# Optimization experiments

Measured on AMD Instinct MI355X. Metric: run time of the kernel, lower is better.

The kernel has to match this reference:

```python
import math
import jax, jax.numpy as jnp
import numpy as np

B, N, D, H, PQ, PV = 2, 2048, 256, 8, 4, 8
HD = D // H
OUT_IN = D + H * PV * 3 + H  # 256 + 192 + 8 = 456


def setup_inputs() -> dict:
    key = jax.random.key(0)
    ks = jax.random.split(key, 12)
    w = lambda k, shape: (jax.random.normal(k, shape, jnp.float32) * 0.02)
    return {
        "x": jax.random.normal(ks[0], (B, N, D), jnp.float32),
        "rotations": jax.random.normal(ks[1], (B, N, 3, 3), jnp.float32),
        "translations": jax.random.normal(ks[2], (B, N, 3), jnp.float32),
        "mask": jnp.ones((B, N), dtype=bool),
        "Wq": w(ks[3], (D, D)), "bq": jnp.zeros((D,), jnp.float32),
        "Wk": w(ks[4], (D, D)), "bk": jnp.zeros((D,), jnp.float32),
        "Wv": w(ks[5], (D, D)), "bv": jnp.zeros((D,), jnp.float32),
        "Wo": w(ks[6], (OUT_IN, D)), "bo": jnp.zeros((D,), jnp.float32),
        "head_weights": jnp.ones((H,), jnp.float32),
    }


def reference(x, rotations, translations, mask, Wq, bq, Wk, bk, Wv, bv, Wo, bo, head_weights):
    b, n, d = x.shape
    h = head_weights.shape[0]
    hd = d // h
    pv3 = Wo.shape[0] - d - h  # num_heads * num_value_points * 3

    q = (x @ Wq + bq).reshape(b, n, h, hd)
    k = (x @ Wk + bk).reshape(b, n, h, hd)
    v = (x @ Wv + bv).reshape(b, n, h, hd)

    # scalar attention logits [b,h,i,j]
    attn_scores = jnp.einsum("bihd,bjhd->bhij", q, k) / math.sqrt(hd)

    # point-distance bias from frame translations (rotated q/k/v points are
    # dead code in the original module and are omitted)
    diff = translations[:, :, None, :] - translations[:, None, :, :]  # [b,i,j,3]
    dist_sq = jnp.sum(diff * diff, axis=-1)                            # [b,i,j]
    point_attn = -0.5 * dist_sq[:, None, :, :]                         # [b,1,i,j]

    weights = jax.nn.softmax(head_weights)                             # [h]
    combined = attn_scores + point_attn * weights[None, :, None, None]
    combined = jnp.where(mask[:, None, None, :], combined, -1e9)
    attn_probs = jax.nn.softmax(combined, axis=-1)                     # [b,h,i,j]

    attn_output = jnp.einsum("bhij,bjhd->bihd", attn_probs, v).reshape(b, n, d)

    # translation-weighted points, brought back to local frame
    trans_weighted = jnp.einsum("bhij,bjc->bihc", attn_probs, translations)  # [b,i,h,3]
    trans_local = trans_weighted - translations[:, :, None, :]
    point_out = trans_local.reshape(b, n, h * 3)
    point_out = jnp.pad(point_out, ((0, 0), (0, 0), (0, pv3 - h * 3)))

    mean_dist = jnp.sqrt(jnp.mean(dist_sq, axis=-1, keepdims=True) + 1e-8)  # [b,n,1]
    pair_features = jnp.broadcast_to(mean_dist, (b, n, h))

    output = jnp.concatenate([attn_output, point_out, pair_features], axis=-1)
    return output @ Wo + bo
```

## Files before the change

### kernel.cpp

```cpp
#include <hip/hip_runtime.h>

typedef unsigned short u16;
typedef __attribute__((ext_vector_type(8))) short bf16x8;
typedef __attribute__((ext_vector_type(4))) float f32x4;
typedef __attribute__((ext_vector_type(16))) float f32x16;
typedef __attribute__((ext_vector_type(4))) unsigned u32x4;

#define NB 2
#define NSEQ 2048
#define DD 256
#define NH 8
#define NTOK 4096
#define KF 288
#define KFP 296
#define NSPLIT 4
#define PS 36
#define TSTR 2048

#define L_V 1024
#define L_A 2048
#define L_U 3072
#define L_ZP 3328
#define L_STR 3344

#define SCL2E 0.25506973f
#define L2E 1.4426950408889634f

__device__ __forceinline__ u16 f2b(float f) {
  unsigned u = __builtin_bit_cast(unsigned, f);
  return (u16)((u + 0x7fffu + ((u >> 16) & 1u)) >> 16);
}

__device__ __forceinline__ unsigned cvt_pk_bf16(float lo, float hi) {
  unsigned r;
  asm("v_cvt_pk_bf16_f32 %0, %1, %2" : "=v"(r) : "v"(lo), "v"(hi));
  return r;
}

__device__ __forceinline__ void permlane32_swap(unsigned& a, unsigned& b) {
  asm volatile("v_permlane32_swap_b32 %0, %1" : "+v"(a), "+v"(b));
}

__device__ __forceinline__ f32x4 mfma16(bf16x8 a, bf16x8 b, f32x4 c) {
  return __builtin_amdgcn_mfma_f32_16x16x32_bf16(a, b, c, 0, 0, 0);
}
__device__ __forceinline__ f32x16 mfma32(bf16x8 a, bf16x8 b, f32x16 c) {
  return __builtin_amdgcn_mfma_f32_32x32x16_bf16(a, b, c, 0, 0, 0);
}

#define PB_XB 1024
#define PB_WT (PB_XB + 264)
#define PB_BS (PB_WT + 2)
#define PB_T4 (PB_BS + 16)
#define PB_UC (PB_T4 + 128)
#define PB_AC (PB_UC + 64)
#define PB_N  (PB_AC + 1)
__global__ __launch_bounds__(256) void prep(
    const float* __restrict__ x, const float* __restrict__ tr,
    const float* __restrict__ hw, const float* __restrict__ bq,
    const float* __restrict__ bk, const float* __restrict__ bv,
    const float* __restrict__ Wq, const float* __restrict__ Wk,
    const float* __restrict__ Wv, const float* __restrict__ Wo,
    u16* __restrict__ xb, u16* __restrict__ WqkvT, u16* __restrict__ WoPT,
    float4* __restrict__ t4, float4* __restrict__ bstat,
    u16* __restrict__ UC, u16* __restrict__ AC,
    float* __restrict__ b_all, float* __restrict__ wsoft) {
  __shared__ float lt[32][33];
  __shared__ float4 red[4];
  const int bid = blockIdx.x, t = threadIdx.x;
  if (bid < PB_XB) {
    const int i4 = bid * 256 + t;
    float4 v = *(const float4*)(x + (size_t)i4 * 4);
    ushort4 o;
    o.x = f2b(v.x); o.y = f2b(v.y); o.z = f2b(v.z); o.w = f2b(v.w);
    *(ushort4*)(xb + (size_t)i4 * 4) = o;
  } else if (bid < PB_WT) {
    const int bw = bid - PB_XB;
    const int r = t >> 3, c4 = (t & 7) * 4;
    if (bw < 192) {
      int mt = bw >> 3, kt = bw & 7;
      int m0 = mt * 32, k0 = kt * 32;
      const float* W = m0 < 256 ? Wq : (m0 < 512 ? Wk : Wv);
      const int mm = m0 & 255;
      float4 v = *(const float4*)(W + (size_t)(k0 + r) * 256 + mm + c4);
      lt[r][c4] = v.x; lt[r][c4 + 1] = v.y; lt[r][c4 + 2] = v.z; lt[r][c4 + 3] = v.w;
      __syncthreads();
      const float s = m0 < 256 ? SCL2E : 1.f;
      ushort4 o;
      o.x = f2b(lt[c4][r] * s); o.y = f2b(lt[c4 + 1][r] * s);
      o.z = f2b(lt[c4 + 2][r] * s); o.w = f2b(lt[c4 + 3][r] * s);
      *(ushort4*)(WqkvT + (size_t)(m0 + r) * 256 + k0 + c4) = o;
    } else {
      int q = bw - 192;
      int nt2 = q / 9, kt = q - nt2 * 9;
      int n0 = nt2 * 32, kk0 = kt * 32;
      int row = (kk0 + r) < 280 ? (kk0 + r) : (kk0 + r + 168);
      float4 v = *(const float4*)(Wo + (size_t)row * 256 + n0 + c4);
      lt[r][c4] = v.x; lt[r][c4 + 1] = v.y; lt[r][c4 + 2] = v.z; lt[r][c4 + 3] = v.w;
      __syncthreads();
      ushort4 o;
      o.x = f2b(lt[c4][r]); o.y = f2b(lt[c4 + 1][r]);
      o.z = f2b(lt[c4 + 2][r]); o.w = f2b(lt[c4 + 3][r]);
      *(ushort4*)(WoPT + (size_t)(n0 + r) * KF + kk0 + c4) = o;
    }
  } else if (bid < PB_BS) {
    const int b = bid - PB_WT;
    float sx = 0.f, sy = 0.f, sz = 0.f, s2 = 0.f;
    for (int j = t; j < NSEQ; j += 256) {
      float a = tr[(size_t)(b * NSEQ + j) * 3];
      float b2 = tr[(size_t)(b * NSEQ + j) * 3 + 1];
      float c = tr[(size_t)(b * NSEQ + j) * 3 + 2];
      sx += a; sy += b2; sz += c; s2 += a * a + b2 * b2 + c * c;
    }
#pragma unroll
    for (int off = 1; off < 64; off <<= 1) {
      sx += __shfl_xor(sx, off); sy += __shfl_xor(sy, off);
      sz += __shfl_xor(sz, off); s2 += __shfl_xor(s2, off);
    }
    if ((t & 63) == 0) red[t >> 6] = make_float4(sx, sy, sz, s2);
    __syncthreads();
    if (t == 0) {
      float4 a = red[0], b1 = red[1], c = red[2], d = red[3];
      bstat[b] = make_float4(a.x + b1.x + c.x + d.x, a.y + b1.y + c.y + d.y,
                             a.z + b1.z + c.z + d.z, a.w + b1.w + c.w + d.w);
    }
  } else if (bid < PB_T4) {
    const int j = (bid - PB_BS) * 256 + t;
    float a = tr[j * 3], b2 = tr[j * 3 + 1], c = tr[j * 3 + 2];
    t4[j] = make_float4(a, b2, c, a * a + b2 * b2 + c * c);
  } else if (bid < PB_UC) {
    const int id = (bid - PB_T4) * 256 + t;
    const int b = id >> 14, jt = (id >> 8) & 63, c = (id >> 3) & 31, e = id & 7;
    const int tok = b * NSEQ + jt * 32 + c;
    float v = 0.f;
    if (e < 3) v = tr[(size_t)tok * 3 + e];
    else if (e == 3) {
      float a = tr[(size_t)tok * 3], b2 = tr[(size_t)tok * 3 + 1],
            cz = tr[(size_t)tok * 3 + 2];
      v = a * a + b2 * b2 + cz * cz;
    } else if (e == 4) v = 1.f;
    UC[id] = f2b(v);
  } else if (bid < PB_AC) {
    const int id = (bid - PB_UC) * 256 + t;
    const int b = id >> 13, jt = (id >> 7) & 63, sub = (id >> 5) & 3,
              cch = (id >> 3) & 3, e = id & 7;
    const int j = jt * 32 + (sub >> 1) * 16 + (sub & 1) * 8 + e;
    float v = cch == 0 ? 1.f : tr[(size_t)(b * NSEQ + j) * 3 + cch - 1];
    AC[id] = f2b(v);
  } else {
    for (int i = t; i < 768; i += 256)
      b_all[i] = i < 256 ? bq[i] * SCL2E : i < 512 ? bk[i - 256] : bv[i - 512];
    if (t == 0) {
      float mx = hw[0];
      for (int i = 1; i < NH; i++) mx = fmaxf(mx, hw[i]);
      float e[NH], sum = 0.f;
      for (int i = 0; i < NH; i++) { e[i] = __expf(hw[i] - mx); sum += e[i]; }
      for (int i = 0; i < NH; i++) wsoft[i] = e[i] / sum;
    }
  }
}

__global__ __launch_bounds__(256) void gemm_qkv(
    const u16* __restrict__ AT, const u16* __restrict__ BT,
    const float* __restrict__ bias, u16* __restrict__ Qb,
    u16* __restrict__ TLB) {
  __shared__ u16 vt[128][65];
  const int lane = threadIdx.x & 63, wv = threadIdx.x >> 6;
  const int il = lane & 15, g = lane >> 4;
  const int wm = wv >> 1, wn = wv & 1;
  const int yb = blockIdx.y;
  const int mblk = yb * 64 + wm * 32;
  const int nblk = blockIdx.x * 128 + wn * 64;
  f32x4 acc[2][4];
#pragma unroll
  for (int a = 0; a < 2; a++)
#pragma unroll
    for (int b = 0; b < 4; b++) acc[a][b] = (f32x4)(0.f);
  const u16* Abase = AT + (size_t)(mblk + il) * DD + 8 * g;
  const u16* Bbase = BT + (size_t)(nblk + il) * DD + 8 * g;
#pragma unroll
  for (int kk = 0; kk < DD; kk += 32) {
    bf16x8 aF[2], bF[4];
#pragma unroll
    for (int mt = 0; mt < 2; mt++)
      aF[mt] = *(const bf16x8*)(Abase + (size_t)mt * 16 * DD + kk);
#pragma unroll
    for (int nt = 0; nt < 4; nt++)
      bF[nt] = *(const bf16x8*)(Bbase + (size_t)nt * 16 * DD + kk);
#pragma unroll
    for (int mt = 0; mt < 2; mt++)
#pragma unroll
      for (int nt = 0; nt < 4; nt++)
        acc[mt][nt] = mfma16(aF[mt], bF[nt], acc[mt][nt]);
  }
#pragma unroll
  for (int nt = 0; nt < 4; nt++) {
    const int n_g = nblk + nt * 16 + il;
#pragma unroll
    for (int mt = 0; mt < 2; mt++) {
      const int m0 = mblk + mt * 16 + 4 * g;
      f32x4 v = acc[mt][nt];
      const float4 bb = *(const float4*)(bias + m0);
      v[0] += bb.x; v[1] += bb.y; v[2] += bb.z; v[3] += bb.w;
      ushort4 u;
      u.x = f2b(v[0]); u.y = f2b(v[1]); u.z = f2b(v[2]); u.w = f2b(v[3]);
      if (yb < 4) {
        *(ushort4*)(Qb + (size_t)n_g * 256 + m0) = u;
      } else if (yb < 8) {
        const int f = m0 - 256;
        const int h = f >> 5, dd = (f & 31) >> 3, e0 = f & 7;
        const int b = n_g >> 11, jj = n_g & 2047;
        const int jt = jj >> 5, c = jj & 31;
        u16* tile = TLB + ((size_t)((b * NH + h) * 64 + jt)) * TSTR;
        *(ushort4*)(tile + (size_t)(dd * 32 + c) * 8 + e0) = u;
      } else {
        const int ml = m0 - yb * 64;
        const int nl = wn * 64 + nt * 16 + il;
        vt[nl][ml] = u.x; vt[nl][ml + 1] = u.y;
        vt[nl][ml + 2] = u.z; vt[nl][ml + 3] = u.w;
      }
    }
  }
  if (yb >= 8) {
    __syncthreads();
#pragma unroll
    for (int ii = 0; ii < 4; ++ii) {
      const int q = threadIdx.x + 256 * ii;
      const int jt_loc = q >> 8, qq = q & 255;
      const int sub = qq >> 6, h_loc = (qq >> 5) & 1, c = qq & 31;
      const int jjb = (sub >> 1) * 16 + (sub & 1) * 8;
      const int row0 = jt_loc * 32 + jjb;
      u16 ov[8];
#pragma unroll
      for (int e = 0; e < 8; e++) ov[e] = vt[row0 + e][h_loc * 32 + c];
      const int tok = blockIdx.x * 128 + row0;
      const int b = tok >> 11, jj = tok & 2047, jt = jj >> 5;
      const int h = (yb - 8) * 2 + h_loc;
      u16* tile = TLB + ((size_t)((b * NH + h) * 64 + jt)) * TSTR + L_V;
      *(bf16x8*)(tile + sub * 256 + c * 8) = *(bf16x8*)ov;
    }
  }
}

__global__ __launch_bounds__(256, 4) void attn_kernel(
    const u16* __restrict__ Qb, const u16* __restrict__ TLB,
    const u16* __restrict__ UC, const u16* __restrict__ AC,
    const float4* __restrict__ t4, const float* __restrict__ wsoft,
    float* __restrict__ part) {
  __shared__ __align__(16) u16 lds[2 * L_STR];
  const int tid = threadIdx.x;
  const int lane = tid & 63, wv = tid >> 6;
  const int c = lane & 31, hi = lane >> 5;
  const int bid = blockIdx.x;
  const int idx = bid >> 3;
  const int c2 = (bid & 7) * 8 + (idx >> 4);
  const int bh = c2 >> 2, s = c2 & 3;
  const int b = bh >> 3, h = bh & 7;
  const int qb = (idx & 15) * 128 + wv * 32;
  const int iglob = b * NSEQ + qb + c;

  const u16* qptr = Qb + (size_t)iglob * 256 + h * 32 + 8 * hi;
  const bf16x8 qf0 = *(const bf16x8*)qptr;
  const bf16x8 qf1 = *(const bf16x8*)(qptr + 16);
  const float4 ti = t4[iglob];
  const float w = wsoft[h];
  const float WD = w * L2E, NH2 = -0.5f * WD;
  u32x4 vw = (u32x4)(0u);
  if (hi == 0) {
    vw[0] = cvt_pk_bf16(WD * ti.x, WD * ti.y);
    vw[1] = cvt_pk_bf16(WD * ti.z, NH2);
    vw[2] = cvt_pk_bf16(NH2 * ti.w, 0.f);
  }
  const bf16x8 vf = __builtin_bit_cast(bf16x8, vw);

  f32x16 o = (f32x16)(0.f), aacc = (f32x16)(0.f);
  const int jt0 = s * 16;
  const u16* tK = TLB + ((size_t)bh * 64 + jt0) * TSTR;
  const u16* tA = AC + ((size_t)b * 64 + jt0) * 128;
  const u16* tU = UC + ((size_t)b * 64 + jt0) * 256;
  const int fo = hi * 256 + c * 8;

  {
    unsigned* zz = (unsigned*)lds;
    for (int i = tid; i < 1296; i += 256) {
      int k = (i < 648) ? (L_A / 2 + i) : (L_STR / 2 + L_A / 2 + i - 648);
      zz[k] = 0;
    }
  }
  __syncthreads();
  bf16x8 gkv = *(const bf16x8*)(tK + (size_t)tid * 8);
  bf16x8 ga, gu;
  if (tid < 16) ga = *(const bf16x8*)(tA + tid * 8);
  else if (tid < 48) gu = *(const bf16x8*)(tU + (tid - 16) * 8);
  *(bf16x8*)(lds + tid * 8) = gkv;
  if (tid < 16) *(bf16x8*)(lds + L_A + (tid >> 2) * 256 + (tid & 3) * 8) = ga;
  else if (tid < 48) *(bf16x8*)(lds + L_U + (tid - 16) * 8) = gu;
  __syncthreads();

#pragma unroll 1
  for (int t = 0; t < 16; ++t) {
    if (t < 15) {
      gkv = *(const bf16x8*)(tK + (size_t)(t + 1) * TSTR + tid * 8);
      if (tid < 16) ga = *(const bf16x8*)(tA + (size_t)(t + 1) * 128 + tid * 8);
      else if (tid < 48)
        gu = *(const bf16x8*)(tU + (size_t)(t + 1) * 256 + (tid - 16) * 8);
    }
    const u16* L = lds + (t & 1) * L_STR;
    bf16x8 k0 = *(const bf16x8*)(L + fo);
    bf16x8 k1 = *(const bf16x8*)(L + 512 + fo);
    bf16x8 v0 = *(const bf16x8*)(L + L_V + fo);
    bf16x8 v1 = *(const bf16x8*)(L + L_V + 512 + fo);
    bf16x8 a0 = *(const bf16x8*)(L + L_A + fo);
    bf16x8 a1 = *(const bf16x8*)(L + L_A + 512 + fo);
    bf16x8 uf = *(const bf16x8*)(hi ? (L + L_ZP) : (L + L_U + c * 8));
    __builtin_amdgcn_s_setprio(1);
    f32x16 sa = mfma32(uf, vf, (f32x16)(0.f));
    sa = mfma32(k0, qf0, sa);
    sa = mfma32(k1, qf1, sa);
    float p[16];
#pragma unroll
    for (int r = 0; r < 16; r++) p[r] = exp2f(sa[r]);
    unsigned x0 = cvt_pk_bf16(p[0], p[1]), y0 = cvt_pk_bf16(p[4], p[5]);
    unsigned z0 = cvt_pk_bf16(p[2], p[3]), w0 = cvt_pk_bf16(p[6], p[7]);
    permlane32_swap(x0, y0);
    permlane32_swap(z0, w0);
    unsigned x1 = cvt_pk_bf16(p[8], p[9]), y1 = cvt_pk_bf16(p[12], p[13]);
    unsigned z1 = cvt_pk_bf16(p[10], p[11]), w1 = cvt_pk_bf16(p[14], p[15]);
    permlane32_swap(x1, y1);
    permlane32_swap(z1, w1);
    bf16x8 pa0 = __builtin_bit_cast(bf16x8, (u32x4){x0, z0, y0, w0});
    bf16x8 pa1 = __builtin_bit_cast(bf16x8, (u32x4){x1, z1, y1, w1});
    o = mfma32(pa0, v0, o);
    o = mfma32(pa1, v1, o);
    aacc = mfma32(pa0, a0, aacc);
    aacc = mfma32(pa1, a1, aacc);
    __builtin_amdgcn_s_setprio(0);
    if (t < 15) {
      u16* D = lds + ((t + 1) & 1) * L_STR;
      *(bf16x8*)(D + tid * 8) = gkv;
      if (tid < 16) *(bf16x8*)(D + L_A + (tid >> 2) * 256 + (tid & 3) * 8) = ga;
      else if (tid < 48) *(bf16x8*)(D + L_U + (tid - 16) * 8) = gu;
    }
    __syncthreads();
  }

  float* pbase = part + ((size_t)(s * 16 + bh) * NSEQ + qb) * PS;
#pragma unroll
  for (int r = 0; r < 16; r++) {
    const int irow = (r & 3) + 8 * (r >> 2) + 4 * hi;
    float* pr = pbase + (size_t)irow * PS;
    pr[c] = o[r];
    if (c < 4) pr[32 + c] = aacc[r];
  }
}

__global__ __launch_bounds__(256) void outk(
    const float* __restrict__ part, const u16* __restrict__ WoPT,
    const float* __restrict__ bo, const float4* __restrict__ t4,
    const float4* __restrict__ bstat, const float* __restrict__ tr,
    float* __restrict__ out) {
  __shared__ __align__(16) u16 feats[16][KFP];
  __shared__ float invl[16][8];
  const int t = threadIdx.x;
  const int tok0 = blockIdx.x * 16;
  const int b = tok0 >> 11;
  const int i0 = tok0 & 2047;
  const size_t SS = (size_t)16 * NSEQ * PS;
  if (t < 128) {
    const int r = t >> 3, hh = t & 7;
    const float* p = part + ((size_t)(b * 8 + hh) * NSEQ + i0 + r) * PS + 32;
    invl[r][hh] = 1.f / (p[0] + p[SS] + p[2 * SS] + p[3 * SS]);
  }
  __syncthreads();
#pragma unroll
  for (int ii = 0; ii < 4; ++ii) {
    const int id = t + 256 * ii;
    const int r = id >> 6, q4 = id & 63;
    const int cc = q4 * 4, hh = q4 >> 3;
    const float* p =
        part + ((size_t)(b * 8 + hh) * NSEQ + i0 + r) * PS + (cc & 31);
    float4 v0 = *(const float4*)p;
    float4 v1 = *(const float4*)(p + SS);
    float4 v2 = *(const float4*)(p + 2 * SS);
    float4 v3 = *(const float4*)(p + 3 * SS);
    const float inv = invl[r][hh];
    ushort4 u;
    u.x = f2b((v0.x + v1.x + v2.x + v3.x) * inv);
    u.y = f2b((v0.y + v1.y + v2.y + v3.y) * inv);
    u.z = f2b((v0.z + v1.z + v2.z + v3.z) * inv);
    u.w = f2b((v0.w + v1.w + v2.w + v3.w) * inv);
    *(ushort4*)(&feats[r][cc]) = u;
  }
  for (int id = t; id < 384; id += 256) {
    const int r = id / 24, cc = id - r * 24;
    const int comp = cc % 3, hh = cc / 3;
    const float* p =
        part + ((size_t)(b * 8 + hh) * NSEQ + i0 + r) * PS + 33 + comp;
    float v = p[0] + p[SS] + p[2 * SS] + p[3 * SS];
    feats[r][256 + cc] =
        f2b(v * invl[r][hh] - tr[(size_t)(tok0 + r) * 3 + comp]);
  }
  if (t < 128) {
    const int r = t >> 3;
    float4 tt = t4[tok0 + r];
    float4 st = bstat[b];
    float sumd = (float)NSEQ * tt.w + st.w -
                 2.f * (tt.x * st.x + tt.y * st.y + tt.z * st.z);
    feats[r][280 + (t & 7)] = f2b(sqrtf(sumd * (1.f / (float)NSEQ) + 1e-8f));
  }
  __syncthreads();
  const int lane = t & 63, wv = t >> 6;
  const int il = lane & 15, g = lane >> 4;
  f32x4 acc[4];
#pragma unroll
  for (int mt = 0; mt < 4; mt++) acc[mt] = (f32x4)(0.f);
  const u16* Ab = WoPT + (size_t)(wv * 64 + il) * KF + 8 * g;
#pragma unroll
  for (int kk = 0; kk < KF; kk += 32) {
    bf16x8 bF = *(const bf16x8*)(&feats[il][kk + 8 * g]);
#pragma unroll
    for (int mt = 0; mt < 4; mt++) {
      bf16x8 aF = *(const bf16x8*)(Ab + (size_t)mt * 16 * KF + kk);
      acc[mt] = mfma16(aF, bF, acc[mt]);
    }
  }
  const int n_g = tok0 + il;
#pragma unroll
  for (int mt = 0; mt < 4; mt++) {
    const int m0 = wv * 64 + mt * 16 + 4 * g;
    f32x4 v = acc[mt];
    const float4 bb = *(const float4*)(bo + m0);
    v[0] += bb.x; v[1] += bb.y; v[2] += bb.z; v[3] += bb.w;
    *(float4*)(out + (size_t)n_g * DD + m0) = make_float4(v[0], v[1], v[2], v[3]);
  }
}

extern "C" void kernel_launch(void* const* d_in, const int* in_sizes, int n_in,
                              void* d_out, int out_size, void* d_ws, size_t ws_size,
                              hipStream_t stream) {
  (void)in_sizes; (void)n_in; (void)out_size; (void)ws_size;
  const float* x  = (const float*)d_in[0];
  const float* tr = (const float*)d_in[2];
  const float* Wq = (const float*)d_in[4];
  const float* bq = (const float*)d_in[5];
  const float* Wk = (const float*)d_in[6];
  const float* bk = (const float*)d_in[7];
  const float* Wv = (const float*)d_in[8];
  const float* bv = (const float*)d_in[9];
  const float* Wo = (const float*)d_in[10];
  const float* bo = (const float*)d_in[11];
  const float* hw = (const float*)d_in[12];
  float* out = (float*)d_out;

  char* p = (char*)d_ws;
  auto alloc = [&](size_t n) { char* r = p; p += (n + 255) & ~(size_t)255; return r; };
  u16* xb      = (u16*)alloc((size_t)NTOK * DD * 2);
  u16* WqkvT   = (u16*)alloc((size_t)768 * DD * 2);
  u16* WoPT    = (u16*)alloc((size_t)DD * KF * 2);
  float4* t4   = (float4*)alloc((size_t)NTOK * 16);
  float* b_all = (float*)alloc(768 * 4);
  float* ws    = (float*)alloc(256);
  float4* bst  = (float4*)alloc(256);
  u16* UC      = (u16*)alloc((size_t)NB * 64 * 256 * 2);
  u16* AC      = (u16*)alloc((size_t)NB * 64 * 128 * 2);
  u16* Qb      = (u16*)alloc((size_t)NTOK * DD * 2);
  u16* TLB     = (u16*)alloc((size_t)NB * NH * 64 * TSTR * 2);
  float* part  = (float*)alloc((size_t)NSPLIT * 16 * NSEQ * PS * 4);

  prep<<<PB_N, 256, 0, stream>>>(x, tr, hw, bq, bk, bv, Wq, Wk, Wv, Wo, xb,
                                 WqkvT, WoPT, t4, bst, UC, AC, b_all, ws);
  gemm_qkv<<<dim3(32, 12), 256, 0, stream>>>(WqkvT, xb, b_all, Qb, TLB);
  attn_kernel<<<1024, 256, 0, stream>>>(Qb, TLB, UC, AC, t4, ws, part);
  outk<<<256, 256, 0, stream>>>(part, WoPT, bo, t4, bst, tr, out);
}
```

Before: 138.9 us.

## Raise grid parallelism: split KV eight ways, smaller QKV tiles, wider output blocks

Measured after the change: 291.6 us. 110% more time.

```diff
diff --git a/kernel.cpp b/kernel.cpp
--- a/kernel.cpp
+++ b/kernel.cpp
@@ -13,7 +13,7 @@
 #define NTOK 4096
 #define KF 288
 #define KFP 296
-#define NSPLIT 4
+#define NSPLIT 8
 #define PS 36
 #define TSTR 2048
 
@@ -164,37 +164,37 @@
     const u16* __restrict__ AT, const u16* __restrict__ BT,
     const float* __restrict__ bias, u16* __restrict__ Qb,
     u16* __restrict__ TLB) {
-  __shared__ u16 vt[128][65];
+  __shared__ u16 vt[64][65];
   const int lane = threadIdx.x & 63, wv = threadIdx.x >> 6;
   const int il = lane & 15, g = lane >> 4;
   const int wm = wv >> 1, wn = wv & 1;
-  const int yb = blockIdx.y;
+  const int yb = blockIdx.y, bx = blockIdx.x;
   const int mblk = yb * 64 + wm * 32;
-  const int nblk = blockIdx.x * 128 + wn * 64;
-  f32x4 acc[2][4];
+  const int nblk = bx * 64 + wn * 32;
+  f32x4 acc[2][2];
 #pragma unroll
   for (int a = 0; a < 2; a++)
 #pragma unroll
-    for (int b = 0; b < 4; b++) acc[a][b] = (f32x4)(0.f);
+    for (int b = 0; b < 2; b++) acc[a][b] = (f32x4)(0.f);
   const u16* Abase = AT + (size_t)(mblk + il) * DD + 8 * g;
   const u16* Bbase = BT + (size_t)(nblk + il) * DD + 8 * g;
 #pragma unroll
   for (int kk = 0; kk < DD; kk += 32) {
-    bf16x8 aF[2], bF[4];
+    bf16x8 aF[2], bF[2];
 #pragma unroll
     for (int mt = 0; mt < 2; mt++)
       aF[mt] = *(const bf16x8*)(Abase + (size_t)mt * 16 * DD + kk);
 #pragma unroll
-    for (int nt = 0; nt < 4; nt++)
+    for (int nt = 0; nt < 2; nt++)
       bF[nt] = *(const bf16x8*)(Bbase + (size_t)nt * 16 * DD + kk);
 #pragma unroll
     for (int mt = 0; mt < 2; mt++)
 #pragma unroll
-      for (int nt = 0; nt < 4; nt++)
+      for (int nt = 0; nt < 2; nt++)
         acc[mt][nt] = mfma16(aF[mt], bF[nt], acc[mt][nt]);
   }
 #pragma unroll
-  for (int nt = 0; nt < 4; nt++) {
+  for (int nt = 0; nt < 2; nt++) {
     const int n_g = nblk + nt * 16 + il;
 #pragma unroll
     for (int mt = 0; mt < 2; mt++) {
@@ -215,7 +215,7 @@
         *(ushort4*)(tile + (size_t)(dd * 32 + c) * 8 + e0) = u;
       } else {
         const int ml = m0 - yb * 64;
-        const int nl = wn * 64 + nt * 16 + il;
+        const int nl = wn * 32 + nt * 16 + il;
         vt[nl][ml] = u.x; vt[nl][ml + 1] = u.y;
         vt[nl][ml + 2] = u.z; vt[nl][ml + 3] = u.w;
       }
@@ -223,26 +223,25 @@
   }
   if (yb >= 8) {
     __syncthreads();
-#pragma unroll
-    for (int ii = 0; ii < 4; ++ii) {
-      const int q = threadIdx.x + 256 * ii;
-      const int jt_loc = q >> 8, qq = q & 255;
-      const int sub = qq >> 6, h_loc = (qq >> 5) & 1, c = qq & 31;
-      const int jjb = (sub >> 1) * 16 + (sub & 1) * 8;
-      const int row0 = jt_loc * 32 + jjb;
+    const int t = threadIdx.x;
+    const int jt_loc = t >> 7, sub = (t >> 5) & 3, c = t & 31;
+    const int jjb = (sub >> 1) * 16 + (sub & 1) * 8;
+    const int row0 = jt_loc * 32 + jjb;
+    const int b = bx >> 5;
+    const int jt = (bx * 2 + jt_loc) & 63;
+#pragma unroll
+    for (int hh = 0; hh < 2; ++hh) {
       u16 ov[8];
 #pragma unroll
-      for (int e = 0; e < 8; e++) ov[e] = vt[row0 + e][h_loc * 32 + c];
-      const int tok = blockIdx.x * 128 + row0;
-      const int b = tok >> 11, jj = tok & 2047, jt = jj >> 5;
-      const int h = (yb - 8) * 2 + h_loc;
+      for (int e = 0; e < 8; e++) ov[e] = vt[row0 + e][hh * 32 + c];
+      const int h = (yb - 8) * 2 + hh;
       u16* tile = TLB + ((size_t)((b * NH + h) * 64 + jt)) * TSTR + L_V;
       *(bf16x8*)(tile + sub * 256 + c * 8) = *(bf16x8*)ov;
     }
   }
 }
 
-__global__ __launch_bounds__(256, 4) void attn_kernel(
+__global__ __launch_bounds__(256, 8) void attn_kernel(
     const u16* __restrict__ Qb, const u16* __restrict__ TLB,
     const u16* __restrict__ UC, const u16* __restrict__ AC,
     const float4* __restrict__ t4, const float* __restrict__ wsoft,
@@ -253,8 +252,8 @@
   const int c = lane & 31, hi = lane >> 5;
   const int bid = blockIdx.x;
   const int idx = bid >> 3;
-  const int c2 = (bid & 7) * 8 + (idx >> 4);
-  const int bh = c2 >> 2, s = c2 & 3;
+  const int c2 = (bid & 7) * 16 + (idx >> 4);
+  const int bh = c2 >> 3, s = c2 & 7;
   const int b = bh >> 3, h = bh & 7;
   const int qb = (idx & 15) * 128 + wv * 32;
   const int iglob = b * NSEQ + qb + c;
@@ -274,7 +273,7 @@
   const bf16x8 vf = __builtin_bit_cast(bf16x8, vw);
 
   f32x16 o = (f32x16)(0.f), aacc = (f32x16)(0.f);
-  const int jt0 = s * 16;
+  const int jt0 = s * (64 / NSPLIT);
   const u16* tK = TLB + ((size_t)bh * 64 + jt0) * TSTR;
   const u16* tA = AC + ((size_t)b * 64 + jt0) * 128;
   const u16* tU = UC + ((size_t)b * 64 + jt0) * 256;
@@ -298,8 +297,8 @@
   __syncthreads();
 
 #pragma unroll 1
-  for (int t = 0; t < 16; ++t) {
-    if (t < 15) {
+  for (int t = 0; t < 64 / NSPLIT; ++t) {
+    if (t < 64 / NSPLIT - 1) {
       gkv = *(const bf16x8*)(tK + (size_t)(t + 1) * TSTR + tid * 8);
       if (tid < 16) ga = *(const bf16x8*)(tA + (size_t)(t + 1) * 128 + tid * 8);
       else if (tid < 48)
@@ -335,7 +334,7 @@
     aacc = mfma32(pa0, a0, aacc);
     aacc = mfma32(pa1, a1, aacc);
     __builtin_amdgcn_s_setprio(0);
-    if (t < 15) {
+    if (t < 64 / NSPLIT - 1) {
       u16* D = lds + ((t + 1) & 1) * L_STR;
       *(bf16x8*)(D + tid * 8) = gkv;
       if (tid < 16) *(bf16x8*)(D + L_A + (tid >> 2) * 256 + (tid & 3) * 8) = ga;
@@ -354,7 +353,7 @@
   }
 }
 
-__global__ __launch_bounds__(256) void outk(
+__global__ __launch_bounds__(1024) void outk(
     const float* __restrict__ part, const u16* __restrict__ WoPT,
     const float* __restrict__ bo, const float4* __restrict__ t4,
     const float4* __restrict__ bstat, const float* __restrict__ tr,
@@ -369,70 +368,65 @@
   if (t < 128) {
     const int r = t >> 3, hh = t & 7;
     const float* p = part + ((size_t)(b * 8 + hh) * NSEQ + i0 + r) * PS + 32;
-    invl[r][hh] = 1.f / (p[0] + p[SS] + p[2 * SS] + p[3 * SS]);
+    float v = 0.f;
+#pragma unroll
+    for (int k = 0; k < NSPLIT; k++) v += p[k * SS];
+    invl[r][hh] = 1.f / v;
   }
   __syncthreads();
-#pragma unroll
-  for (int ii = 0; ii < 4; ++ii) {
-    const int id = t + 256 * ii;
-    const int r = id >> 6, q4 = id & 63;
+  {
+    const int r = t >> 6, q4 = t & 63;
     const int cc = q4 * 4, hh = q4 >> 3;
     const float* p =
         part + ((size_t)(b * 8 + hh) * NSEQ + i0 + r) * PS + (cc & 31);
-    float4 v0 = *(const float4*)p;
-    float4 v1 = *(const float4*)(p + SS);
-    float4 v2 = *(const float4*)(p + 2 * SS);
-    float4 v3 = *(const float4*)(p + 3 * SS);
+    float4 acc4 = make_float4(0.f, 0.f, 0.f, 0.f);
+#pragma unroll
+    for (int k = 0; k < NSPLIT; k++) {
+      float4 v = *(const float4*)(p + k * SS);
+      acc4.x += v.x; acc4.y += v.y; acc4.z += v.z; acc4.w += v.w;
+    }
     const float inv = invl[r][hh];
     ushort4 u;
-    u.x = f2b((v0.x + v1.x + v2.x + v3.x) * inv);
-    u.y = f2b((v0.y + v1.y + v2.y + v3.y) * inv);
-    u.z = f2b((v0.z + v1.z + v2.z + v3.z) * inv);
-    u.w = f2b((v0.w + v1.w + v2.w + v3.w) * inv);
+    u.x = f2b(acc4.x * inv); u.y = f2b(acc4.y * inv);
+    u.z = f2b(acc4.z * inv); u.w = f2b(acc4.w * inv);
     *(ushort4*)(&feats[r][cc]) = u;
   }
-  for (int id = t; id < 384; id += 256) {
-    const int r = id / 24, cc = id - r * 24;
+  if (t < 384) {
+    const int r = t / 24, cc = t - r * 24;
     const int comp = cc % 3, hh = cc / 3;
     const float* p =
         part + ((size_t)(b * 8 + hh) * NSEQ + i0 + r) * PS + 33 + comp;
-    float v = p[0] + p[SS] + p[2 * SS] + p[3 * SS];
+    float v = 0.f;
+#pragma unroll
+    for (int k = 0; k < NSPLIT; k++) v += p[k * SS];
     feats[r][256 + cc] =
         f2b(v * invl[r][hh] - tr[(size_t)(tok0 + r) * 3 + comp]);
-  }
-  if (t < 128) {
-    const int r = t >> 3;
-    float4 tt = t4[tok0 + r];
+  } else if (t >= 512 && t < 640) {
+    const int tt = t - 512;
+    const int r = tt >> 3;
+    float4 t4v = t4[tok0 + r];
     float4 st = bstat[b];
-    float sumd = (float)NSEQ * tt.w + st.w -
-                 2.f * (tt.x * st.x + tt.y * st.y + tt.z * st.z);
-    feats[r][280 + (t & 7)] = f2b(sqrtf(sumd * (1.f / (float)NSEQ) + 1e-8f));
+    float sumd = (float)NSEQ * t4v.w + st.w -
+                 2.f * (t4v.x * st.x + t4v.y * st.y + t4v.z * st.z);
+    feats[r][280 + (tt & 7)] = f2b(sqrtf(sumd * (1.f / (float)NSEQ) + 1e-8f));
   }
   __syncthreads();
-  const int lane = t & 63, wv = t >> 6;
+  const int lane = t & 63, w = t >> 6;
   const int il = lane & 15, g = lane >> 4;
-  f32x4 acc[4];
-#pragma unroll
-  for (int mt = 0; mt < 4; mt++) acc[mt] = (f32x4)(0.f);
-  const u16* Ab = WoPT + (size_t)(wv * 64 + il) * KF + 8 * g;
+  f32x4 acc = (f32x4)(0.f);
+  const u16* Ab = WoPT + (size_t)(w * 16 + il) * KF + 8 * g;
 #pragma unroll
   for (int kk = 0; kk < KF; kk += 32) {
     bf16x8 bF = *(const bf16x8*)(&feats[il][kk + 8 * g]);
-#pragma unroll
-    for (int mt = 0; mt < 4; mt++) {
-      bf16x8 aF = *(const bf16x8*)(Ab + (size_t)mt * 16 * KF + kk);
-      acc[mt] = mfma16(aF, bF, acc[mt]);
-    }
+    bf16x8 aF = *(const bf16x8*)(Ab + kk);
+    acc = mfma16(aF, bF, acc);
   }
   const int n_g = tok0 + il;
-#pragma unroll
-  for (int mt = 0; mt < 4; mt++) {
-    const int m0 = wv * 64 + mt * 16 + 4 * g;
-    f32x4 v = acc[mt];
-    const float4 bb = *(const float4*)(bo + m0);
-    v[0] += bb.x; v[1] += bb.y; v[2] += bb.z; v[3] += bb.w;
-    *(float4*)(out + (size_t)n_g * DD + m0) = make_float4(v[0], v[1], v[2], v[3]);
-  }
+  const int m0 = w * 16 + 4 * g;
+  const float4 bb = *(const float4*)(bo + m0);
+  acc[0] += bb.x; acc[1] += bb.y; acc[2] += bb.z; acc[3] += bb.w;
+  *(float4*)(out + (size_t)n_g * DD + m0) =
+      make_float4(acc[0], acc[1], acc[2], acc[3]);
 }
 
 extern "C" void kernel_launch(void* const* d_in, const int* in_sizes, int n_in,
@@ -469,7 +463,7 @@
 
   prep<<<PB_N, 256, 0, stream>>>(x, tr, hw, bq, bk, bv, Wq, Wk, Wv, Wo, xb,
                                  WqkvT, WoPT, t4, bst, UC, AC, b_all, ws);
-  gemm_qkv<<<dim3(32, 12), 256, 0, stream>>>(WqkvT, xb, b_all, Qb, TLB);
-  attn_kernel<<<1024, 256, 0, stream>>>(Qb, TLB, UC, AC, t4, ws, part);
-  outk<<<256, 256, 0, stream>>>(part, WoPT, bo, t4, bst, tr, out);
-}
+  gemm_qkv<<<dim3(64, 12), 256, 0, stream>>>(WqkvT, xb, b_all, Qb, TLB);
+  attn_kernel<<<2048, 256, 0, stream>>>(Qb, TLB, UC, AC, t4, ws, part);
+  outk<<<256, 1024, 0, stream>>>(part, WoPT, bo, t4, bst, tr, out);
+}
```
